# Kernel tuning notes

Hardware: AMD Instinct MI355X
Metric: run time of the kernel (lower is better)

Reference implementation:

```python
import jax, jax.numpy as jnp
import numpy as np

S1 = (42, 1600, 1408); S2 = (21, 800, 704); S3 = (11, 400, 352); S4 = (6, 200, 176)
OFF = np.array([[dz, dy, dx] for dz in (-1, 0, 1) for dy in (-1, 0, 1) for dx in (-1, 0, 1)], np.int64)
KOFF = np.array([[kz, ky, kx] for kz in (0, 1, 2) for ky in (0, 1, 2) for kx in (0, 1, 2)], np.int64)

def _keys(c, s):
    return (c[:, 0] * s[1] + c[:, 1]) * s[2] + c[:, 2]

def _lookup(skeys, qk, valid):
    pos = np.searchsorted(skeys, qk)
    posc = np.clip(pos, 0, len(skeys) - 1)
    found = valid & (skeys[posc] == qk)
    return np.where(found, posc, -1).astype(np.int32)

def _subm_nbr(coords, skeys, shape):
    N = len(coords); nbr = np.empty((N, 27), np.int32); sh = np.array(shape)
    for t in range(27):
        q = coords + OFF[t]
        valid = np.all((q >= 0) & (q < sh), axis=1)
        nbr[:, t] = _lookup(skeys, _keys(q, shape), valid)
    return nbr

def _inv_nbr(fcoords, ckeys, cshape):
    # inverse of stride-2, pad-1, k-3 sparse conv: coarse = (fine + 1 - k) / 2
    N = len(fcoords); nbr = np.empty((N, 27), np.int32); csh = np.array(cshape)
    for t in range(27):
        cand = fcoords + 1 - KOFF[t]
        valid = np.all(cand >= 0, axis=1) & np.all(cand % 2 == 0, axis=1)
        cc = cand // 2
        valid &= np.all(cc < csh, axis=1)
        nbr[:, t] = _lookup(ckeys, _keys(cc, cshape), valid)
    return nbr

def _geometry():
    rng = np.random.default_rng(0)
    n = 130000
    c = np.stack([rng.integers(0, S1[i], n) for i in range(3)], 1).astype(np.int64)
    uk, idx = np.unique(_keys(c, S1), return_index=True)
    c1 = c[idx][:100000]; k1 = uk[:len(c1)]
    def down(cf, s):
        cc = cf // 2
        uk, idx = np.unique(_keys(cc, s), return_index=True)
        return cc[idx], uk
    c2, k2 = down(c1, S2); c3, k3 = down(c2, S3); c4, k4 = down(c3, S4)
    return dict(nbr4=_subm_nbr(c4, k4, S4), inv43=_inv_nbr(c3, k4, S4),
                nbr3=_subm_nbr(c3, k3, S3), inv32=_inv_nbr(c2, k3, S3),
                nbr2=_subm_nbr(c2, k2, S2), inv21=_inv_nbr(c1, k2, S2),
                nbr1=_subm_nbr(c1, k1, S1), n4=len(c4), n1=len(c1))

_SPECS = [("m4", 64, 64), ("i4", 64, 64), ("m3", 64, 64), ("i3", 64, 32),
          ("m2", 32, 32), ("i2", 32, 16), ("m1", 16, 16), ("c5", 16, 3)]

def _params(key):
    p = {}
    for i, (nm, ci, co) in enumerate(_SPECS):
        k = jax.random.fold_in(key, i)
        p["W_" + nm] = jax.random.normal(k, (27, ci, co), jnp.float32) * (1.0 / np.sqrt(27.0 * ci))
        p["g_" + nm] = jnp.ones((co,), jnp.float32)
        p["b_" + nm] = jnp.zeros((co,), jnp.float32)
    return p

def setup_inputs() -> dict:
    geo = _geometry()
    key = jax.random.key(0)
    inp = {k: jnp.asarray(v) for k, v in geo.items() if k.startswith(("nbr", "inv"))}
    inp["x"] = jax.random.normal(jax.random.fold_in(key, 100), (geo["n4"], 64), jnp.float32)
    inp.update(_params(key))
    return inp

def _block(f, nbr, W, g, b, relu=True):
    # gather-GEMM (sparse conv), then BatchNorm1d (training mode, eps=1e-3), then ReLU
    m = nbr >= 0                                             # [N,27]
    x = jnp.where(m[..., None], f[jnp.maximum(nbr, 0)], 0.0)  # [N,27,Cin]
    y = jnp.einsum('nkc,kcd->nd', x, W)                      # [N,Cout]
    mu = y.mean(0); var = y.var(0)
    y = (y - mu) * jax.lax.rsqrt(var + 1e-3) * g + b
    return jax.nn.relu(y) if relu else y

def reference(x, nbr4, inv43, nbr3, inv32, nbr2, inv21, nbr1,
              W_m4, g_m4, b_m4, W_i4, g_i4, b_i4, W_m3, g_m3, b_m3, W_i3, g_i3, b_i3,
              W_m2, g_m2, b_m2, W_i2, g_i2, b_i2, W_m1, g_m1, b_m1, W_c5, g_c5, b_c5):
    h = _block(x, nbr4, W_m4, g_m4, b_m4)      # subm4: [N4,64]
    h = _block(h, inv43, W_i4, g_i4, b_i4)     # inverse conv4 -> [N3,64]
    h = _block(h, nbr3, W_m3, g_m3, b_m3)      # subm3
    h = _block(h, inv32, W_i3, g_i3, b_i3)     # inverse conv3 -> [N2,32]
    h = _block(h, nbr2, W_m2, g_m2, b_m2)      # subm2
    h = _block(h, inv21, W_i2, g_i2, b_i2)     # inverse conv2 -> [N1,16]
    h = _block(h, nbr1, W_m1, g_m1, b_m1)      # subm1
    return _block(h, nbr1, W_c5, g_c5, b_c5, relu=False)  # conv5 (shares subm1 rulebook), BN only
```

## Files before the change

### kernel.cpp

```cpp
#include <hip/hip_runtime.h>

typedef _Float16 HALF;
typedef _Float16 f16x8 __attribute__((ext_vector_type(8)));
typedef float f32x4 __attribute__((ext_vector_type(4)));
typedef int i32x4 __attribute__((ext_vector_type(4)));

struct WArgs { const float* W[8]; HALF* dst[8]; };

__global__ void convert_all_w_kernel(WArgs a)
{
    const int CIs[8]  = {64, 64, 64, 64, 32, 32, 16, 16};
    const int COs[8]  = {64, 64, 64, 32, 32, 16, 16, 3};
    const int COPs[8] = {64, 64, 64, 32, 32, 16, 16, 16};
    const int L = blockIdx.y;
    const int CI = CIs[L], CO = COs[L], COP = COPs[L];
    const int K = 27 * CI, KP = (K + 31) & ~31;
    const int total = COP * KP;
    for (int i = blockIdx.x * 256 + threadIdx.x; i < total; i += gridDim.x * 256) {
        int jp = i / KP;
        int kp = i - jp * KP;
        float v = (jp < CO && kp < K) ? a.W[L][(size_t)kp * CO + jp] : 0.f;
        a.dst[L][((size_t)(kp >> 5) * COP + jp) * 32 + (kp & 31)] = (HALF)v;
    }
}

__global__ void convert_x_kernel(const float* __restrict__ x, HALF* __restrict__ xh, int total)
{
    int i = blockIdx.x * 256 + threadIdx.x;
    if (i < total) xh[i] = (HALF)x[i];
}

template<int CI, int CO_PAD, int NMT, bool FUSED>
__global__ __launch_bounds__(256, 2) void conv_kernel(
    const HALF* __restrict__ h, const int* __restrict__ nbr,
    const HALF* __restrict__ Wt, HALF* __restrict__ yout,
    float* __restrict__ sums, int n,
    const float* __restrict__ psums, const float* __restrict__ pg,
    const float* __restrict__ pb, float pinvn)
{
    constexpr int K    = 27 * CI;
    constexpr int KP   = (K + 31) & ~31;
    constexpr int NCH  = KP / 32;
    constexpr int NJB  = CO_PAD / 16;
    constexpr int NW   = 4;
    constexpr int NCB  = (CI >= 64) ? 2 : 1;
    constexpr int LOG2CI = (CI == 64) ? 6 : ((CI == 32) ? 5 : 4);
    constexpr int NIDX = (CI == 16) ? 14 : 27;

    __shared__ float red[2][NW][CO_PAD];

    const int wv   = threadIdx.x >> 6;
    const int lane = threadIdx.x & 63;
    const int l15  = lane & 15;
    const int lq   = lane >> 4;
    const int waveRow = blockIdx.x * (NW * 16 * NMT) + wv * (16 * NMT);

    f32x4 acc[NMT][NJB];
#pragma unroll
    for (int mt = 0; mt < NMT; ++mt)
#pragma unroll
        for (int jb = 0; jb < NJB; ++jb)
#pragma unroll
            for (int r = 0; r < 4; ++r) acc[mt][jb][r] = 0.f;

    int idxr[NMT][NIDX];
#pragma unroll
    for (int mt = 0; mt < NMT; ++mt) {
        const int row  = waveRow + mt * 16 + l15;
        const bool rok = row < n;
        const int* nb  = nbr + (size_t)min(row, n - 1) * 27;
#pragma unroll
        for (int s = 0; s < NIDX; ++s) {
            const int t = (CI == 16) ? (2 * s + (lq >> 1)) : s;
            const int v = nb[t < 27 ? t : 26];
            idxr[mt][s] = (rok && t < 27) ? v : -1;
        }
    }

    f16x8 sc8[NCB], bi8[NCB];
    if constexpr (FUSED) {
#pragma unroll
        for (int cb = 0; cb < NCB; ++cb) {
            const int c0 = cb * 32 + ((lq * 8) & (CI - 1));
#pragma unroll
            for (int j = 0; j < 8; ++j) {
                const int c = c0 + j;
                const float mu  = psums[c] * pinvn;
                const float var = psums[CI + c] * pinvn - mu * mu;
                const float sc  = rsqrtf(var + 1e-3f) * pg[c];
                sc8[cb][j] = (HALF)sc;
                bi8[cb][j] = (HALF)(pb[c] - mu * sc);
            }
        }
    }

#pragma unroll
    for (int kc = 0; kc < NCH; ++kc) {
        const int c   = (kc * 32 + lq * 8) & (CI - 1);
        const int slot = (CI == 64) ? (kc >> 1) : kc;
        const int ccb  = (NCB == 2) ? (kc & 1) : 0;

        const HALF* wb = Wt + (size_t)kc * (CO_PAD * 32) + lq * 8;
        f16x8 b[NJB];
#pragma unroll
        for (int jb = 0; jb < NJB; ++jb)
            b[jb] = *(const f16x8*)(wb + (size_t)(jb * 16 + l15) * 32);

#pragma unroll
        for (int mt = 0; mt < NMT; ++mt) {
            const int idx = idxr[mt][slot];
            const int off = (max(idx, 0) << LOG2CI) + c;
            f16x8 a = *(const f16x8*)(h + off);
            if constexpr (FUSED) {
                a = a * sc8[ccb] + bi8[ccb];
#pragma unroll
                for (int j = 0; j < 8; ++j)
                    a[j] = (a[j] < (HALF)0.f) ? (HALF)0.f : a[j];
            }
            const int m = ~(idx >> 31);
            i32x4 ai = __builtin_bit_cast(i32x4, a);
            ai.x &= m; ai.y &= m; ai.z &= m; ai.w &= m;
            a = __builtin_bit_cast(f16x8, ai);
#pragma unroll
            for (int jb = 0; jb < NJB; ++jb)
                acc[mt][jb] = __builtin_amdgcn_mfma_f32_16x16x32_f16(a, b[jb], acc[mt][jb], 0, 0, 0);
        }
    }

#pragma unroll
    for (int jb = 0; jb < NJB; ++jb) {
        const int col = jb * 16 + l15;
        float s = 0.f, sq = 0.f;
#pragma unroll
        for (int mt = 0; mt < NMT; ++mt) {
            const int rb = waveRow + mt * 16 + lq * 4;
#pragma unroll
            for (int r = 0; r < 4; ++r) {
                if (rb + r < n) {
                    const float v = acc[mt][jb][r];
                    yout[(size_t)(rb + r) * CO_PAD + col] = (HALF)v;
                    s += v;
                    sq += v * v;
                }
            }
        }
        s  += __shfl_xor(s, 16);  s  += __shfl_xor(s, 32);
        sq += __shfl_xor(sq, 16); sq += __shfl_xor(sq, 32);
        if (lane < 16) { red[0][wv][col] = s; red[1][wv][col] = sq; }
    }
    __syncthreads();
    if (threadIdx.x < CO_PAD) {
        float s = 0.f, sq = 0.f;
#pragma unroll
        for (int w = 0; w < NW; ++w) { s += red[0][w][threadIdx.x]; sq += red[1][w][threadIdx.x]; }
        atomicAdd(&sums[threadIdx.x], s);
        atomicAdd(&sums[CO_PAD + threadIdx.x], sq);
    }
}

__global__ void bn_out_kernel(const HALF* __restrict__ y, const float* __restrict__ sums,
                              const float* __restrict__ g, const float* __restrict__ b,
                              int n, float invn, float* __restrict__ out)
{
    int i = blockIdx.x * 256 + threadIdx.x;
    if (i >= n * 3) return;
    int row = i / 3;
    int c = i - row * 3;
    float mu  = sums[c] * invn;
    float var = sums[16 + c] * invn - mu * mu;
    float sc  = rsqrtf(var + 1e-3f) * g[c];
    out[i] = ((float)y[(size_t)row * 16 + c] - mu) * sc + b[c];
}

extern "C" void kernel_launch(void* const* d_in, const int* in_sizes, int n_in,
                              void* d_out, int out_size, void* d_ws, size_t ws_size,
                              hipStream_t stream)
{
    const int* nbr4  = (const int*)d_in[0];
    const int* inv43 = (const int*)d_in[1];
    const int* nbr3  = (const int*)d_in[2];
    const int* inv32 = (const int*)d_in[3];
    const int* nbr2  = (const int*)d_in[4];
    const int* inv21 = (const int*)d_in[5];
    const int* nbr1  = (const int*)d_in[6];
    const float* x   = (const float*)d_in[7];

    const int n4 = in_sizes[0] / 27;
    const int n3 = in_sizes[1] / 27;
    const int n2 = in_sizes[3] / 27;
    const int n1 = in_sizes[5] / 27;

    const int CIs[8]  = {64, 64, 64, 64, 32, 32, 16, 16};
    const int COPs[8] = {64, 64, 64, 32, 32, 16, 16, 16};
    int KPs[8], wtoff[8];
    int wtot = 0;
    for (int s = 0; s < 8; ++s) {
        KPs[s] = ((27 * CIs[s] + 31) / 32) * 32;
        wtoff[s] = wtot;
        wtot += COPs[s] * KPs[s];
    }

    char* ws = (char*)d_ws;
    HALF* wt = (HALF*)ws;
    size_t off = ((size_t)wtot * sizeof(HALF) + 255) & ~(size_t)255;
    float* sums = (float*)(ws + off);
    off += 8 * 128 * sizeof(float);
    off = (off + 255) & ~(size_t)255;
    HALF* xh = (HALF*)(ws + off);
    off += ((size_t)n4 * 64 * sizeof(HALF) + 255) & ~(size_t)255;
    size_t bufElems = 0;
    {
        size_t cand[4] = {(size_t)n4 * 64, (size_t)n3 * 64, (size_t)n2 * 32, (size_t)n1 * 16};
        for (int i = 0; i < 4; ++i) if (cand[i] > bufElems) bufElems = cand[i];
    }
    HALF* Y0 = (HALF*)(ws + off);
    off += (bufElems * sizeof(HALF) + 255) & ~(size_t)255;
    HALF* Y1 = (HALF*)(ws + off);

    hipMemsetAsync(sums, 0, 8 * 128 * sizeof(float), stream);

    WArgs wa;
    for (int s = 0; s < 8; ++s) { wa.W[s] = (const float*)d_in[8 + 3 * s]; wa.dst[s] = wt + wtoff[s]; }
    {
        int maxTotal = 64 * KPs[0];
        dim3 grid((maxTotal + 255) / 256, 8);
        convert_all_w_kernel<<<grid, 256, 0, stream>>>(wa);
    }
    convert_x_kernel<<<(n4 * 64 + 255) / 256, 256, 0, stream>>>(x, xh, n4 * 64);

#define G(s) ((const float*)d_in[9 + 3 * (s)])
#define B(s) ((const float*)d_in[10 + 3 * (s)])
#define SUMS(s) (sums + (s) * 128)
#define GRID(nn) (((nn) + 127) / 128)

    conv_kernel<64, 64, 2, false><<<GRID(n4), 256, 0, stream>>>(
        xh, nbr4, wt + wtoff[0], Y0, SUMS(0), n4, nullptr, nullptr, nullptr, 0.f);
    conv_kernel<64, 64, 2, true><<<GRID(n3), 256, 0, stream>>>(
        Y0, inv43, wt + wtoff[1], Y1, SUMS(1), n3, SUMS(0), G(0), B(0), 1.f / n4);
    conv_kernel<64, 64, 2, true><<<GRID(n3), 256, 0, stream>>>(
        Y1, nbr3, wt + wtoff[2], Y0, SUMS(2), n3, SUMS(1), G(1), B(1), 1.f / n3);
    conv_kernel<64, 32, 2, true><<<GRID(n2), 256, 0, stream>>>(
        Y0, inv32, wt + wtoff[3], Y1, SUMS(3), n2, SUMS(2), G(2), B(2), 1.f / n3);
    conv_kernel<32, 32, 2, true><<<GRID(n2), 256, 0, stream>>>(
        Y1, nbr2, wt + wtoff[4], Y0, SUMS(4), n2, SUMS(3), G(3), B(3), 1.f / n2);
    conv_kernel<32, 16, 2, true><<<GRID(n1), 256, 0, stream>>>(
        Y0, inv21, wt + wtoff[5], Y1, SUMS(5), n1, SUMS(4), G(4), B(4), 1.f / n2);
    conv_kernel<16, 16, 2, true><<<GRID(n1), 256, 0, stream>>>(
        Y1, nbr1, wt + wtoff[6], Y0, SUMS(6), n1, SUMS(5), G(5), B(5), 1.f / n1);
    conv_kernel<16, 16, 2, true><<<GRID(n1), 256, 0, stream>>>(
        Y0, nbr1, wt + wtoff[7], Y1, SUMS(7), n1, SUMS(6), G(6), B(6), 1.f / n1);
    bn_out_kernel<<<(n1 * 3 + 255) / 256, 256, 0, stream>>>(
        Y1, SUMS(7), G(7), B(7), n1, 1.f / n1, (float*)d_out);

#undef G
#undef B
#undef SUMS
#undef GRID
}
```

Measured before the change: 569.7 us.

## Use 32x32x16 MFMA conv kernel with register prefetch for wider layers

```diff
diff --git a/kernel.cpp b/kernel.cpp
--- a/kernel.cpp
+++ b/kernel.cpp
@@ -3,6 +3,7 @@
 typedef _Float16 HALF;
 typedef _Float16 f16x8 __attribute__((ext_vector_type(8)));
 typedef float f32x4 __attribute__((ext_vector_type(4)));
+typedef float f32x16 __attribute__((ext_vector_type(16)));
 typedef int i32x4 __attribute__((ext_vector_type(4)));
 
 struct WArgs { const float* W[8]; HALF* dst[8]; };
@@ -12,15 +13,16 @@
     const int CIs[8]  = {64, 64, 64, 64, 32, 32, 16, 16};
     const int COs[8]  = {64, 64, 64, 32, 32, 16, 16, 3};
     const int COPs[8] = {64, 64, 64, 32, 32, 16, 16, 16};
+    const int TGs[8]  = {16, 16, 16, 16, 16, 32, 32, 32};
     const int L = blockIdx.y;
-    const int CI = CIs[L], CO = COs[L], COP = COPs[L];
+    const int CI = CIs[L], CO = COs[L], COP = COPs[L], TG = TGs[L];
     const int K = 27 * CI, KP = (K + 31) & ~31;
     const int total = COP * KP;
     for (int i = blockIdx.x * 256 + threadIdx.x; i < total; i += gridDim.x * 256) {
         int jp = i / KP;
         int kp = i - jp * KP;
         float v = (jp < CO && kp < K) ? a.W[L][(size_t)kp * CO + jp] : 0.f;
-        a.dst[L][((size_t)(kp >> 5) * COP + jp) * 32 + (kp & 31)] = (HALF)v;
+        a.dst[L][((size_t)(kp / TG) * COP + jp) * TG + (kp % TG)] = (HALF)v;
     }
 }
 
@@ -28,6 +30,154 @@
 {
     int i = blockIdx.x * 256 + threadIdx.x;
     if (i < total) xh[i] = (HALF)x[i];
+}
+
+template<int CI, int CO_PAD, int NMT, bool FUSED>
+__global__ __launch_bounds__(256, 2) void conv32_kernel(
+    const HALF* __restrict__ h, const int* __restrict__ nbr,
+    const HALF* __restrict__ Wt, HALF* __restrict__ yout,
+    float* __restrict__ sums, int n,
+    const float* __restrict__ psums, const float* __restrict__ pg,
+    const float* __restrict__ pb, float pinvn)
+{
+    constexpr int K    = 27 * CI;
+    constexpr int NCH  = K / 16;
+    constexpr int NJB  = CO_PAD / 32;
+    constexpr int NW   = 4;
+    constexpr int LOG2CI = (CI == 64) ? 6 : 5;
+    constexpr int CPT  = CI / 16;
+    constexpr int NCB  = CPT;
+
+    __shared__ float red[2][NW][CO_PAD];
+
+    const int wv   = threadIdx.x >> 6;
+    const int lane = threadIdx.x & 63;
+    const int l31  = lane & 31;
+    const int lq2  = lane >> 5;
+    const int waveRow = blockIdx.x * (NW * 32 * NMT) + wv * (32 * NMT);
+
+    f32x16 acc[NMT][NJB];
+#pragma unroll
+    for (int mt = 0; mt < NMT; ++mt)
+#pragma unroll
+        for (int jb = 0; jb < NJB; ++jb)
+#pragma unroll
+            for (int r = 0; r < 16; ++r) acc[mt][jb][r] = 0.f;
+
+    int idxr[NMT][27];
+#pragma unroll
+    for (int mt = 0; mt < NMT; ++mt) {
+        const int row  = waveRow + mt * 32 + l31;
+        const bool rok = row < n;
+        const int* nb  = nbr + (size_t)min(row, n - 1) * 27;
+#pragma unroll
+        for (int t = 0; t < 27; ++t) {
+            const int v = nb[t];
+            idxr[mt][t] = rok ? v : -1;
+        }
+    }
+
+    f16x8 sc8[NCB], bi8[NCB];
+    if constexpr (FUSED) {
+#pragma unroll
+        for (int cb = 0; cb < NCB; ++cb) {
+            const int c0 = cb * 16 + (lq2 << 3);
+#pragma unroll
+            for (int j = 0; j < 8; ++j) {
+                const int c = c0 + j;
+                const float mu  = psums[c] * pinvn;
+                const float var = psums[CI + c] * pinvn - mu * mu;
+                const float sc  = rsqrtf(var + 1e-3f) * pg[c];
+                sc8[cb][j] = (HALF)sc;
+                bi8[cb][j] = (HALF)(pb[c] - mu * sc);
+            }
+        }
+    }
+
+    f16x8 aC[NMT], bC[NJB];
+    int   iC[NMT];
+#pragma unroll
+    for (int mt = 0; mt < NMT; ++mt) {
+        const int idx = idxr[mt][0];
+        iC[mt] = idx;
+        aC[mt] = *(const f16x8*)(h + (max(idx, 0) << LOG2CI) + (lq2 << 3));
+    }
+#pragma unroll
+    for (int jb = 0; jb < NJB; ++jb)
+        bC[jb] = *(const f16x8*)(Wt + (size_t)(jb * 32 + l31) * 16 + (lq2 << 3));
+
+#pragma unroll
+    for (int kc = 0; kc < NCH; ++kc) {
+        f16x8 aN[NMT], bN[NJB];
+        int   iN[NMT];
+        if (kc + 1 < NCH) {
+            const int slot = (kc + 1) / CPT;
+            const int c    = ((kc + 1) % CPT) * 16 + (lq2 << 3);
+#pragma unroll
+            for (int mt = 0; mt < NMT; ++mt) {
+                const int idx = idxr[mt][slot];
+                iN[mt] = idx;
+                aN[mt] = *(const f16x8*)(h + (max(idx, 0) << LOG2CI) + c);
+            }
+#pragma unroll
+            for (int jb = 0; jb < NJB; ++jb)
+                bN[jb] = *(const f16x8*)(Wt + ((size_t)(kc + 1) * CO_PAD + jb * 32 + l31) * 16 + (lq2 << 3));
+        }
+
+        const int ccb = kc % CPT;
+#pragma unroll
+        for (int mt = 0; mt < NMT; ++mt) {
+            f16x8 a = aC[mt];
+            if constexpr (FUSED) {
+                a = a * sc8[ccb] + bi8[ccb];
+#pragma unroll
+                for (int j = 0; j < 8; ++j)
+                    a[j] = (a[j] < (HALF)0.f) ? (HALF)0.f : a[j];
+            }
+            const int m = ~(iC[mt] >> 31);
+            i32x4 ai = __builtin_bit_cast(i32x4, a);
+            ai.x &= m; ai.y &= m; ai.z &= m; ai.w &= m;
+            a = __builtin_bit_cast(f16x8, ai);
+#pragma unroll
+            for (int jb = 0; jb < NJB; ++jb)
+                acc[mt][jb] = __builtin_amdgcn_mfma_f32_32x32x16_f16(a, bC[jb], acc[mt][jb], 0, 0, 0);
+        }
+        if (kc + 1 < NCH) {
+#pragma unroll
+            for (int mt = 0; mt < NMT; ++mt) { aC[mt] = aN[mt]; iC[mt] = iN[mt]; }
+#pragma unroll
+            for (int jb = 0; jb < NJB; ++jb) bC[jb] = bN[jb];
+        }
+    }
+
+#pragma unroll
+    for (int jb = 0; jb < NJB; ++jb) {
+        const int col = jb * 32 + l31;
+        float s = 0.f, sq = 0.f;
+#pragma unroll
+        for (int mt = 0; mt < NMT; ++mt) {
+#pragma unroll
+            for (int r = 0; r < 16; ++r) {
+                const int row = waveRow + mt * 32 + (r & 3) + 8 * (r >> 2) + 4 * lq2;
+                if (row < n) {
+                    const float v = acc[mt][jb][r];
+                    yout[(size_t)row * CO_PAD + col] = (HALF)v;
+                    s += v;
+                    sq += v * v;
+                }
+            }
+        }
+        s += __shfl_xor(s, 32); sq += __shfl_xor(sq, 32);
+        if (lane < 32) { red[0][wv][col] = s; red[1][wv][col] = sq; }
+    }
+    __syncthreads();
+    if (threadIdx.x < CO_PAD) {
+        float s = 0.f, sq = 0.f;
+#pragma unroll
+        for (int w = 0; w < NW; ++w) { s += red[0][w][threadIdx.x]; sq += red[1][w][threadIdx.x]; }
+        atomicAdd(&sums[threadIdx.x], s);
+        atomicAdd(&sums[CO_PAD + threadIdx.x], sq);
+    }
 }
 
 template<int CI, int CO_PAD, int NMT, bool FUSED>
@@ -96,7 +246,7 @@
 
 #pragma unroll
     for (int kc = 0; kc < NCH; ++kc) {
-        const int c   = (kc * 32 + lq * 8) & (CI - 1);
+        const int c    = (kc * 32 + lq * 8) & (CI - 1);
         const int slot = (CI == 64) ? (kc >> 1) : kc;
         const int ccb  = (NCB == 2) ? (kc & 1) : 0;
 
@@ -231,23 +381,24 @@
 #define G(s) ((const float*)d_in[9 + 3 * (s)])
 #define B(s) ((const float*)d_in[10 + 3 * (s)])
 #define SUMS(s) (sums + (s) * 128)
-#define GRID(nn) (((nn) + 127) / 128)
-
-    conv_kernel<64, 64, 2, false><<<GRID(n4), 256, 0, stream>>>(
+#define GRID32(nn) (((nn) + 255) / 256)
+#define GRID16(nn) (((nn) + 127) / 128)
+
+    conv32_kernel<64, 64, 2, false><<<GRID32(n4), 256, 0, stream>>>(
         xh, nbr4, wt + wtoff[0], Y0, SUMS(0), n4, nullptr, nullptr, nullptr, 0.f);
-    conv_kernel<64, 64, 2, true><<<GRID(n3), 256, 0, stream>>>(
+    conv32_kernel<64, 64, 2, true><<<GRID32(n3), 256, 0, stream>>>(
         Y0, inv43, wt + wtoff[1], Y1, SUMS(1), n3, SUMS(0), G(0), B(0), 1.f / n4);
-    conv_kernel<64, 64, 2, true><<<GRID(n3), 256, 0, stream>>>(
+    conv32_kernel<64, 64, 2, true><<<GRID32(n3), 256, 0, stream>>>(
         Y1, nbr3, wt + wtoff[2], Y0, SUMS(2), n3, SUMS(1), G(1), B(1), 1.f / n3);
-    conv_kernel<64, 32, 2, true><<<GRID(n2), 256, 0, stream>>>(
+    conv32_kernel<64, 32, 2, true><<<GRID32(n2), 256, 0, stream>>>(
         Y0, inv32, wt + wtoff[3], Y1, SUMS(3), n2, SUMS(2), G(2), B(2), 1.f / n3);
-    conv_kernel<32, 32, 2, true><<<GRID(n2), 256, 0, stream>>>(
+    conv32_kernel<32, 32, 2, true><<<GRID32(n2), 256, 0, stream>>>(
         Y1, nbr2, wt + wtoff[4], Y0, SUMS(4), n2, SUMS(3), G(3), B(3), 1.f / n2);
-    conv_kernel<32, 16, 2, true><<<GRID(n1), 256, 0, stream>>>(
+    conv_kernel<32, 16, 2, true><<<GRID16(n1), 256, 0, stream>>>(
         Y0, inv21, wt + wtoff[5], Y1, SUMS(5), n1, SUMS(4), G(4), B(4), 1.f / n2);
-    conv_kernel<16, 16, 2, true><<<GRID(n1), 256, 0, stream>>>(
+    conv_kernel<16, 16, 2, true><<<GRID16(n1), 256, 0, stream>>>(
         Y1, nbr1, wt + wtoff[6], Y0, SUMS(6), n1, SUMS(5), G(5), B(5), 1.f / n1);
-    conv_kernel<16, 16, 2, true><<<GRID(n1), 256, 0, stream>>>(
+    conv_kernel<16, 16, 2, true><<<GRID16(n1), 256, 0, stream>>>(
         Y0, nbr1, wt + wtoff[7], Y1, SUMS(7), n1, SUMS(6), G(6), B(6), 1.f / n1);
     bn_out_kernel<<<(n1 * 3 + 255) / 256, 256, 0, stream>>>(
         Y1, SUMS(7), G(7), B(7), n1, 1.f / n1, (float*)d_out);
@@ -255,5 +406,6 @@
 #undef G
 #undef B
 #undef SUMS
-#undef GRID
-}
+#undef GRID32
+#undef GRID16
+}
```

After: 1.559 ms. 2.74x slower.

## Stage weights in double-buffered LDS and replace neighbor masking with sentinel row

Applied to the files above, without the earlier changes.

```diff
diff --git a/kernel.cpp b/kernel.cpp
--- a/kernel.cpp
+++ b/kernel.cpp
@@ -3,7 +3,6 @@
 typedef _Float16 HALF;
 typedef _Float16 f16x8 __attribute__((ext_vector_type(8)));
 typedef float f32x4 __attribute__((ext_vector_type(4)));
-typedef int i32x4 __attribute__((ext_vector_type(4)));
 
 struct WArgs { const float* W[8]; HALF* dst[8]; };
 
@@ -14,46 +13,60 @@
     const int COPs[8] = {64, 64, 64, 32, 32, 16, 16, 16};
     const int L = blockIdx.y;
     const int CI = CIs[L], CO = COs[L], COP = COPs[L];
-    const int K = 27 * CI, KP = (K + 31) & ~31;
-    const int total = COP * KP;
-    for (int i = blockIdx.x * 256 + threadIdx.x; i < total; i += gridDim.x * 256) {
-        int jp = i / KP;
-        int kp = i - jp * KP;
-        float v = (jp < CO && kp < K) ? a.W[L][(size_t)kp * CO + jp] : 0.f;
-        a.dst[L][((size_t)(kp >> 5) * COP + jp) * 32 + (kp & 31)] = (HALF)v;
-    }
-}
-
-__global__ void convert_x_kernel(const float* __restrict__ x, HALF* __restrict__ xh, int total)
+    const int K = 27 * CI, KP = (K + 31) & ~31, NCH = KP / 32, NJB = COP / 16;
+    const int total = NCH * NJB * 512;
+    for (int e = blockIdx.x * 256 + threadIdx.x; e < total; e += gridDim.x * 256) {
+        const int j    = e & 7;
+        const int u    = e >> 3;
+        const int lane = u & 63;
+        const int q    = u >> 6;
+        const int jb   = q % NJB;
+        const int kc   = q / NJB;
+        const int k    = kc * 32 + (lane >> 4) * 8 + j;
+        const int co   = jb * 16 + (lane & 15);
+        const float v  = (k < K && co < CO) ? a.W[L][(size_t)k * CO + co] : 0.f;
+        a.dst[L][e] = (HALF)v;
+    }
+}
+
+__global__ void convert_x_kernel(const float* __restrict__ x, HALF* __restrict__ xh,
+                                 int total, int pad)
 {
     int i = blockIdx.x * 256 + threadIdx.x;
     if (i < total) xh[i] = (HALF)x[i];
-}
-
-template<int CI, int CO_PAD, int NMT, bool FUSED>
+    else if (i < total + pad) xh[i] = (HALF)0.f;
+}
+
+template<int CI, int CO_PAD, int GRP, bool FUSED>
 __global__ __launch_bounds__(256, 2) void conv_kernel(
     const HALF* __restrict__ h, const int* __restrict__ nbr,
     const HALF* __restrict__ Wt, HALF* __restrict__ yout,
-    float* __restrict__ sums, int n,
+    float* __restrict__ sums, int* __restrict__ counter, int n, int hn,
     const float* __restrict__ psums, const float* __restrict__ pg,
-    const float* __restrict__ pb, float pinvn)
+    const float* __restrict__ pb, float pinvn,
+    const float* __restrict__ og, const float* __restrict__ ob, float oinvn)
 {
     constexpr int K    = 27 * CI;
     constexpr int KP   = (K + 31) & ~31;
     constexpr int NCH  = KP / 32;
     constexpr int NJB  = CO_PAD / 16;
-    constexpr int NW   = 4;
-    constexpr int NCB  = (CI >= 64) ? 2 : 1;
+    constexpr int NMT  = 2;
+    constexpr int NG   = (NCH + GRP - 1) / GRP;
     constexpr int LOG2CI = (CI == 64) ? 6 : ((CI == 32) ? 5 : 4);
     constexpr int NIDX = (CI == 16) ? 14 : 27;
-
-    __shared__ float red[2][NW][CO_PAD];
-
-    const int wv   = threadIdx.x >> 6;
-    const int lane = threadIdx.x & 63;
+    constexpr int NCB  = (CI == 64) ? 2 : 1;
+    constexpr int SITER = GRP * NJB * 64 / 256;
+
+    __shared__ __align__(16) HALF bst[2][GRP * NJB * 512];
+    __shared__ float red[2][4][CO_PAD];
+    __shared__ int isLast;
+
+    const int tid  = threadIdx.x;
+    const int wv   = tid >> 6;
+    const int lane = tid & 63;
     const int l15  = lane & 15;
     const int lq   = lane >> 4;
-    const int waveRow = blockIdx.x * (NW * 16 * NMT) + wv * (16 * NMT);
+    const int waveRow = blockIdx.x * 128 + wv * 32;
 
     f32x4 acc[NMT][NJB];
 #pragma unroll
@@ -68,12 +81,13 @@
     for (int mt = 0; mt < NMT; ++mt) {
         const int row  = waveRow + mt * 16 + l15;
         const bool rok = row < n;
-        const int* nb  = nbr + (size_t)min(row, n - 1) * 27;
+        const int* nb  = nbr + (size_t)(rok ? row : (n - 1)) * 27;
 #pragma unroll
         for (int s = 0; s < NIDX; ++s) {
             const int t = (CI == 16) ? (2 * s + (lq >> 1)) : s;
             const int v = nb[t < 27 ? t : 26];
-            idxr[mt][s] = (rok && t < 27) ? v : -1;
+            const int id = (rok && t < 27 && v >= 0) ? v : hn;
+            idxr[mt][s] = id << LOG2CI;
         }
     }
 
@@ -94,37 +108,58 @@
         }
     }
 
-#pragma unroll
-    for (int kc = 0; kc < NCH; ++kc) {
-        const int c   = (kc * 32 + lq * 8) & (CI - 1);
-        const int slot = (CI == 64) ? (kc >> 1) : kc;
-        const int ccb  = (NCB == 2) ? (kc & 1) : 0;
-
-        const HALF* wb = Wt + (size_t)kc * (CO_PAD * 32) + lq * 8;
-        f16x8 b[NJB];
-#pragma unroll
-        for (int jb = 0; jb < NJB; ++jb)
-            b[jb] = *(const f16x8*)(wb + (size_t)(jb * 16 + l15) * 32);
-
-#pragma unroll
-        for (int mt = 0; mt < NMT; ++mt) {
-            const int idx = idxr[mt][slot];
-            const int off = (max(idx, 0) << LOG2CI) + c;
-            f16x8 a = *(const f16x8*)(h + off);
-            if constexpr (FUSED) {
-                a = a * sc8[ccb] + bi8[ccb];
-#pragma unroll
-                for (int j = 0; j < 8; ++j)
-                    a[j] = (a[j] < (HALF)0.f) ? (HALF)0.f : a[j];
+    {
+        f16x8 stg[SITER];
+#pragma unroll
+        for (int i = 0; i < SITER; ++i)
+            stg[i] = *(const f16x8*)(Wt + ((size_t)i * 256 + tid) * 8);
+#pragma unroll
+        for (int i = 0; i < SITER; ++i)
+            *(f16x8*)&bst[0][((size_t)i * 256 + tid) * 8] = stg[i];
+    }
+    __syncthreads();
+
+#pragma unroll
+    for (int g = 0; g < NG; ++g) {
+        f16x8 stg[SITER];
+        if (g + 1 < NG) {
+            const HALF* gs = Wt + (size_t)(g + 1) * GRP * NJB * 512 + (size_t)tid * 8;
+#pragma unroll
+            for (int i = 0; i < SITER; ++i)
+                stg[i] = *(const f16x8*)(gs + (size_t)i * 2048);
+        }
+#pragma unroll
+        for (int ki = 0; ki < GRP; ++ki) {
+            if (g * GRP + ki < NCH) {
+                const int kc = g * GRP + ki;
+                f16x8 b[NJB];
+#pragma unroll
+                for (int jb = 0; jb < NJB; ++jb)
+                    b[jb] = *(const f16x8*)&bst[g & 1][((ki * NJB + jb) * 64 + lane) * 8];
+                const int c    = (kc * 32 + lq * 8) & (CI - 1);
+                const int slot = (CI == 64) ? (kc >> 1) : kc;
+                const int ccb  = (NCB == 2) ? (kc & 1) : 0;
+#pragma unroll
+                for (int mt = 0; mt < NMT; ++mt) {
+                    f16x8 a = *(const f16x8*)(h + idxr[mt][slot] + c);
+                    if constexpr (FUSED) {
+                        a = a * sc8[ccb] + bi8[ccb];
+#pragma unroll
+                        for (int j = 0; j < 8; ++j)
+                            a[j] = (a[j] < (HALF)0.f) ? (HALF)0.f : a[j];
+                    }
+#pragma unroll
+                    for (int jb = 0; jb < NJB; ++jb)
+                        acc[mt][jb] = __builtin_amdgcn_mfma_f32_16x16x32_f16(a, b[jb], acc[mt][jb], 0, 0, 0);
+                }
             }
-            const int m = ~(idx >> 31);
-            i32x4 ai = __builtin_bit_cast(i32x4, a);
-            ai.x &= m; ai.y &= m; ai.z &= m; ai.w &= m;
-            a = __builtin_bit_cast(f16x8, ai);
-#pragma unroll
-            for (int jb = 0; jb < NJB; ++jb)
-                acc[mt][jb] = __builtin_amdgcn_mfma_f32_16x16x32_f16(a, b[jb], acc[mt][jb], 0, 0, 0);
-        }
+        }
+        if (g + 1 < NG) {
+#pragma unroll
+            for (int i = 0; i < SITER; ++i)
+                *(f16x8*)&bst[(g + 1) & 1][((size_t)i * 256 + tid) * 8] = stg[i];
+        }
+        __syncthreads();
     }
 
 #pragma unroll
@@ -149,12 +184,26 @@
         if (lane < 16) { red[0][wv][col] = s; red[1][wv][col] = sq; }
     }
     __syncthreads();
-    if (threadIdx.x < CO_PAD) {
+    if (tid < CO_PAD) {
         float s = 0.f, sq = 0.f;
 #pragma unroll
-        for (int w = 0; w < NW; ++w) { s += red[0][w][threadIdx.x]; sq += red[1][w][threadIdx.x]; }
-        atomicAdd(&sums[threadIdx.x], s);
-        atomicAdd(&sums[CO_PAD + threadIdx.x], sq);
+        for (int w = 0; w < 4; ++w) { s += red[0][w][tid]; sq += red[1][w][tid]; }
+        atomicAdd(&sums[tid], s);
+        atomicAdd(&sums[CO_PAD + tid], sq);
+    }
+    __threadfence();
+    __syncthreads();
+    if (tid == 0) isLast = (atomicAdd(counter, 1) == (int)gridDim.x - 1) ? 1 : 0;
+    __syncthreads();
+    if (isLast && tid < CO_PAD) {
+        const float s  = atomicAdd(&sums[tid], 0.f);
+        const float sq = atomicAdd(&sums[CO_PAD + tid], 0.f);
+        const float mu  = s * oinvn;
+        const float var = sq * oinvn - mu * mu;
+        const float sc  = rsqrtf(var + 1e-3f) * og[tid];
+        const float bi  = ob[tid] - mu * sc;
+        const float sent = (fabsf(sc) > 1e-20f) ? (-bi / sc) : 0.f;
+        yout[(size_t)n * CO_PAD + tid] = (HALF)sent;
     }
 }
 
@@ -192,63 +241,74 @@
 
     const int CIs[8]  = {64, 64, 64, 64, 32, 32, 16, 16};
     const int COPs[8] = {64, 64, 64, 32, 32, 16, 16, 16};
-    int KPs[8], wtoff[8];
+    const int GRPs[8] = {6, 6, 6, 8, 8, 8, 8, 8};
+    int wtoff[8];
     int wtot = 0;
     for (int s = 0; s < 8; ++s) {
-        KPs[s] = ((27 * CIs[s] + 31) / 32) * 32;
+        int KP  = ((27 * CIs[s] + 31) / 32) * 32;
+        int NCH = KP / 32;
+        int NG  = (NCH + GRPs[s] - 1) / GRPs[s];
         wtoff[s] = wtot;
-        wtot += COPs[s] * KPs[s];
+        wtot += NG * GRPs[s] * COPs[s] * 32;
     }
 
     char* ws = (char*)d_ws;
     HALF* wt = (HALF*)ws;
     size_t off = ((size_t)wtot * sizeof(HALF) + 255) & ~(size_t)255;
     float* sums = (float*)(ws + off);
-    off += 8 * 128 * sizeof(float);
+    int* counters = (int*)(ws + off + 8 * 128 * sizeof(float));
+    off += 8 * 128 * sizeof(float) + 8 * sizeof(int);
     off = (off + 255) & ~(size_t)255;
     HALF* xh = (HALF*)(ws + off);
-    off += ((size_t)n4 * 64 * sizeof(HALF) + 255) & ~(size_t)255;
-    size_t bufElems = 0;
+    off += (((size_t)n4 * 64 + 64) * sizeof(HALF) + 255) & ~(size_t)255;
+    size_t bufElems = 64;
     {
         size_t cand[4] = {(size_t)n4 * 64, (size_t)n3 * 64, (size_t)n2 * 32, (size_t)n1 * 16};
-        for (int i = 0; i < 4; ++i) if (cand[i] > bufElems) bufElems = cand[i];
+        for (int i = 0; i < 4; ++i) if (cand[i] + 64 > bufElems) bufElems = cand[i] + 64;
     }
     HALF* Y0 = (HALF*)(ws + off);
     off += (bufElems * sizeof(HALF) + 255) & ~(size_t)255;
     HALF* Y1 = (HALF*)(ws + off);
 
-    hipMemsetAsync(sums, 0, 8 * 128 * sizeof(float), stream);
+    hipMemsetAsync(sums, 0, 8 * 128 * sizeof(float) + 8 * sizeof(int), stream);
 
     WArgs wa;
     for (int s = 0; s < 8; ++s) { wa.W[s] = (const float*)d_in[8 + 3 * s]; wa.dst[s] = wt + wtoff[s]; }
     {
-        int maxTotal = 64 * KPs[0];
-        dim3 grid((maxTotal + 255) / 256, 8);
+        dim3 grid(432, 8);
         convert_all_w_kernel<<<grid, 256, 0, stream>>>(wa);
     }
-    convert_x_kernel<<<(n4 * 64 + 255) / 256, 256, 0, stream>>>(x, xh, n4 * 64);
+    convert_x_kernel<<<(n4 * 64 + 64 + 255) / 256, 256, 0, stream>>>(x, xh, n4 * 64, 64);
 
 #define G(s) ((const float*)d_in[9 + 3 * (s)])
 #define B(s) ((const float*)d_in[10 + 3 * (s)])
 #define SUMS(s) (sums + (s) * 128)
 #define GRID(nn) (((nn) + 127) / 128)
 
-    conv_kernel<64, 64, 2, false><<<GRID(n4), 256, 0, stream>>>(
-        xh, nbr4, wt + wtoff[0], Y0, SUMS(0), n4, nullptr, nullptr, nullptr, 0.f);
-    conv_kernel<64, 64, 2, true><<<GRID(n3), 256, 0, stream>>>(
-        Y0, inv43, wt + wtoff[1], Y1, SUMS(1), n3, SUMS(0), G(0), B(0), 1.f / n4);
-    conv_kernel<64, 64, 2, true><<<GRID(n3), 256, 0, stream>>>(
-        Y1, nbr3, wt + wtoff[2], Y0, SUMS(2), n3, SUMS(1), G(1), B(1), 1.f / n3);
-    conv_kernel<64, 32, 2, true><<<GRID(n2), 256, 0, stream>>>(
-        Y0, inv32, wt + wtoff[3], Y1, SUMS(3), n2, SUMS(2), G(2), B(2), 1.f / n3);
-    conv_kernel<32, 32, 2, true><<<GRID(n2), 256, 0, stream>>>(
-        Y1, nbr2, wt + wtoff[4], Y0, SUMS(4), n2, SUMS(3), G(3), B(3), 1.f / n2);
-    conv_kernel<32, 16, 2, true><<<GRID(n1), 256, 0, stream>>>(
-        Y0, inv21, wt + wtoff[5], Y1, SUMS(5), n1, SUMS(4), G(4), B(4), 1.f / n2);
-    conv_kernel<16, 16, 2, true><<<GRID(n1), 256, 0, stream>>>(
-        Y1, nbr1, wt + wtoff[6], Y0, SUMS(6), n1, SUMS(5), G(5), B(5), 1.f / n1);
-    conv_kernel<16, 16, 2, true><<<GRID(n1), 256, 0, stream>>>(
-        Y0, nbr1, wt + wtoff[7], Y1, SUMS(7), n1, SUMS(6), G(6), B(6), 1.f / n1);
+    conv_kernel<64, 64, 6, false><<<GRID(n4), 256, 0, stream>>>(
+        xh, nbr4, wt + wtoff[0], Y0, SUMS(0), counters + 0, n4, n4,
+        nullptr, nullptr, nullptr, 0.f, G(0), B(0), 1.f / n4);
+    conv_kernel<64, 64, 6, true><<<GRID(n3), 256, 0, stream>>>(
+        Y0, inv43, wt + wtoff[1], Y1, SUMS(1), counters + 1, n3, n4,
+        SUMS(0), G(0), B(0), 1.f / n4, G(1), B(1), 1.f / n3);
+    conv_kernel<64, 64, 6, true><<<GRID(n3), 256, 0, stream>>>(
+        Y1, nbr3, wt + wtoff[2], Y0, SUMS(2), counters + 2, n3, n3,
+        SUMS(1), G(1), B(1), 1.f / n3, G(2), B(2), 1.f / n3);
+    conv_kernel<64, 32, 8, true><<<GRID(n2), 256, 0, stream>>>(
+        Y0, inv32, wt + wtoff[3], Y1, SUMS(3), counters + 3, n2, n3,
+        SUMS(2), G(2), B(2), 1.f / n3, G(3), B(3), 1.f / n2);
+    conv_kernel<32, 32, 8, true><<<GRID(n2), 256, 0, stream>>>(
+        Y1, nbr2, wt + wtoff[4], Y0, SUMS(4), counters + 4, n2, n2,
+        SUMS(3), G(3), B(3), 1.f / n2, G(4), B(4), 1.f / n2);
+    conv_kernel<32, 16, 8, true><<<GRID(n1), 256, 0, stream>>>(
+        Y0, inv21, wt + wtoff[5], Y1, SUMS(5), counters + 5, n1, n2,
+        SUMS(4), G(4), B(4), 1.f / n2, G(5), B(5), 1.f / n1);
+    conv_kernel<16, 16, 8, true><<<GRID(n1), 256, 0, stream>>>(
+        Y1, nbr1, wt + wtoff[6], Y0, SUMS(6), counters + 6, n1, n1,
+        SUMS(5), G(5), B(5), 1.f / n1, G(6), B(6), 1.f / n1);
+    conv_kernel<16, 16, 8, true><<<GRID(n1), 256, 0, stream>>>(
+        Y0, nbr1, wt + wtoff[7], Y1, SUMS(7), counters + 7, n1, n1,
+        SUMS(6), G(6), B(6), 1.f / n1, G(7), B(7), 1.f / n1);
     bn_out_kernel<<<(n1 * 3 + 255) / 256, 256, 0, stream>>>(
         Y1, SUMS(7), G(7), B(7), n1, 1.f / n1, (float*)d_out);
 
```

After: 1.058 ms. +85.6%, slower.
